# Kernel optimization log

Hardware: AMD Instinct MI355X
Metric: run time of the kernel (lower is better)

Reference implementation:

```python
import jax, jax.numpy as jnp
import numpy as np

B, T, N, D, H, K, L = 16, 32, 128, 128, 128, 2, 2
M = K + 1  # one support (laplacian) * K diffusion steps + identity


def setup_inputs() -> dict:
    key = jax.random.key(0)
    ks = jax.random.split(key, 8)
    std = 0.05
    Din = D + H  # layer-0 concat dim (== H+H for layer 1 since D==H)
    return {
        "inputs": jax.random.normal(ks[0], (B, T, N, D), jnp.float32),
        "initial_hidden_state": jnp.zeros((L, B, N * H), jnp.float32),
        # row-stochastic-ish dynamic supports, scaled for stable diffusion
        "supports": jax.random.uniform(ks[1], (1, T, N, N), jnp.float32) / N,
        "Wg0": jax.random.normal(ks[2], (Din * M, 2 * H), jnp.float32) * std,
        "bg0": jnp.ones((2 * H,), jnp.float32),  # bias_start=1.0 for gates
        "Wc0": jax.random.normal(ks[3], (Din * M, H), jnp.float32) * std,
        "bc0": jnp.zeros((H,), jnp.float32),
        "Wg1": jax.random.normal(ks[4], ((H + H) * M, 2 * H), jnp.float32) * std,
        "bg1": jnp.ones((2 * H,), jnp.float32),
        "Wc1": jax.random.normal(ks[5], ((H + H) * M, H), jnp.float32) * std,
        "bc1": jnp.zeros((H,), jnp.float32),
    }


def _dconv(sup, x, W, b):
    """Diffusion graph conv. sup: [S,N,N]; x: [B,N,Dcat] -> [B,N,out].
    Chebyshev recurrence x2 = 2*S@x1 - x0, per the original DCGRU cell.
    Feature layout matches torch code: last axis is (Dcat, num_matrices)."""
    xs = [x]
    for s in range(sup.shape[0]):
        x0 = x
        x1 = jnp.einsum('mn,bnd->bmd', sup[s], x)
        xs.append(x1)
        for _ in range(2, K + 1):
            x2 = 2.0 * jnp.einsum('mn,bnd->bmd', sup[s], x1) - x0
            xs.append(x2)
            x0, x1 = x1, x2
    xc = jnp.stack(xs, axis=-1).reshape(x.shape[0], x.shape[1], -1)  # [B,N,Dcat*M]
    return jnp.einsum('bnd,do->bno', xc, W) + b


def _dcgru_forward(inputs, initial_hidden_state, supports, params):
    # inputs: [B,T,N,D] -> [T,B,N*D]
    x_seq = jnp.transpose(inputs, (1, 0, 2, 3)).reshape(T, B, N * D)
    sup_seq = jnp.transpose(supports, (1, 0, 2, 3))  # [T,S,N,N]
    cur = x_seq
    finals = []
    for i in range(L):
        Wg, bg, Wc, bc = params[i]

        def step(h, xt_sup, Wg=Wg, bg=bg, Wc=Wc, bc=bc):
            xt, sup = xt_sup
            xin = xt.reshape(B, N, -1)
            hm = h.reshape(B, N, H)
            gates = jax.nn.sigmoid(_dconv(sup, jnp.concatenate([xin, hm], -1), Wg, bg))
            r, u = jnp.split(gates, 2, axis=-1)
            c = jnp.tanh(_dconv(sup, jnp.concatenate([xin, r * hm], -1), Wc, bc))
            hn = (u * hm + (1.0 - u) * c).reshape(B, N * H)
            return hn, hn

        h_last, outs = jax.lax.scan(step, initial_hidden_state[i], (cur, sup_seq))
        finals.append(h_last)
        cur = outs
    return jnp.stack(finals, axis=0), cur  # ([L,B,N*H], [T,B,N*H])


def reference(inputs, initial_hidden_state, supports,
              Wg0, bg0, Wc0, bc0, Wg1, bg1, Wc1, bc1):
    params = [(Wg0, bg0, Wc0, bc0), (Wg1, bg1, Wc1, bc1)]
    return _dcgru_forward(inputs, initial_hidden_state, supports, params)
```

## Files before the change

### kernel.cpp

```cpp
#include <hip/hip_runtime.h>
#include <math.h>


typedef __attribute__((ext_vector_type(8))) short bf16x8;
typedef __attribute__((ext_vector_type(4))) float f32x4;

namespace {
constexpr int GD = 256, NTHR = 1024;
constexpr int CTW = 136;
constexpr int BFW = 776;
}

__device__ __forceinline__ unsigned short f2bf(float x) {
  unsigned u = __float_as_uint(x);
  u += 0x7fff + ((u >> 16) & 1);
  return (unsigned short)(u >> 16);
}
__device__ __forceinline__ float bf2f(unsigned hw) {
  return __uint_as_float(hw << 16);
}

__device__ __forceinline__ void grid_barrier(unsigned* bar) {
  __syncthreads();
  if (threadIdx.x == 0) {
    unsigned* cnt = bar;
    unsigned* gen = bar + 32;
    unsigned g = __hip_atomic_load(gen, __ATOMIC_RELAXED, __HIP_MEMORY_SCOPE_AGENT);
    unsigned a = __hip_atomic_fetch_add(cnt, 1u, __ATOMIC_ACQ_REL, __HIP_MEMORY_SCOPE_AGENT);
    if (a == (unsigned)(GD - 1)) {
      __hip_atomic_store(cnt, 0u, __ATOMIC_RELAXED, __HIP_MEMORY_SCOPE_AGENT);
      __hip_atomic_fetch_add(gen, 1u, __ATOMIC_ACQ_REL, __HIP_MEMORY_SCOPE_AGENT);
    } else {
      while (__hip_atomic_load(gen, __ATOMIC_ACQUIRE, __HIP_MEMORY_SCOPE_AGENT) == g) {
        __builtin_amdgcn_s_sleep(1);
      }
    }
  }
  __syncthreads();
}

__device__ __forceinline__ void diffusion(
    int bid, int tid, int s, const float* __restrict__ inputs,
    const float* __restrict__ seqs, const float* __restrict__ hsrc_base,
    const unsigned short* __restrict__ Sfr,
    unsigned short* __restrict__ D1g, unsigned short* __restrict__ D2g,
    unsigned short* lds) {
  const int layer = bid >> 7;
  const int t = layer ? (s - 1) : s;
  const bool act = layer ? (s >= 1) : (s < 32);
  if (!act) return;
  const int b = (bid >> 3) & 15, fs = (bid & 7) * 32;
  const int lane = tid & 63, w = tid >> 6, quad = lane >> 4, l16 = lane & 15;
  unsigned short* catT = lds;
  unsigned short* D1T  = lds + 32 * CTW;

  for (int p = tid; p < 2048; p += NTHR) {
    const int f = p & 31, n2 = (p >> 5) << 1;
    float v0, v1;
    if (fs < 128) {
      const float* xb = (layer == 0)
          ? inputs + (long)((b * 32 + t) * 128) * 128
          : seqs + (long)(t & 1) * 262144 + (long)(b * 128) * 128;
      v0 = xb[n2 * 128 + fs + f];
      v1 = xb[(n2 + 1) * 128 + fs + f];
    } else {
      const float* hb = hsrc_base + (long)(layer * 2048 + b * 128) * 128;
      v0 = hb[n2 * 128 + (fs - 128) + f];
      v1 = hb[(n2 + 1) * 128 + (fs - 128) + f];
    }
    *(unsigned*)(catT + f * CTW + n2) =
        (unsigned)f2bf(v0) | ((unsigned)f2bf(v1) << 16);
  }
  __syncthreads();

  const int mt = w >> 1, ft = w & 1;
  const unsigned short* Sb = Sfr + (long)t * 16384;

  f32x4 acc = {0.f, 0.f, 0.f, 0.f};
#pragma unroll
  for (int ks = 0; ks < 4; ks++) {
    bf16x8 a = *(const bf16x8*)(Sb + (((mt * 4 + ks) * 64) + lane) * 8);
    bf16x8 bb = *(const bf16x8*)(catT + (ft * 16 + l16) * CTW + ks * 32 + quad * 8);
    acc = __builtin_amdgcn_mfma_f32_16x16x32_bf16(a, bb, acc, 0, 0, 0);
  }
  {
    unsigned short* dst = D1T + (ft * 16 + l16) * CTW + mt * 16 + quad * 4;
    const unsigned lo = (unsigned)f2bf(acc[0]) | ((unsigned)f2bf(acc[1]) << 16);
    const unsigned hi = (unsigned)f2bf(acc[2]) | ((unsigned)f2bf(acc[3]) << 16);
    *(uint2*)dst = make_uint2(lo, hi);
  }
  __syncthreads();

  f32x4 acc2 = {0.f, 0.f, 0.f, 0.f};
#pragma unroll
  for (int ks = 0; ks < 4; ks++) {
    bf16x8 a = *(const bf16x8*)(Sb + (((mt * 4 + ks) * 64) + lane) * 8);
    bf16x8 bb = *(const bf16x8*)(D1T + (ft * 16 + l16) * CTW + ks * 32 + quad * 8);
    acc2 = __builtin_amdgcn_mfma_f32_16x16x32_bf16(a, bb, acc2, 0, 0, 0);
  }
  {
    unsigned short* cp = catT + (ft * 16 + l16) * CTW + mt * 16 + quad * 4;
    const uint2 cv = *(const uint2*)cp;
    const float d0 = 2.f * acc2[0] - bf2f(cv.x & 0xffffu);
    const float d1 = 2.f * acc2[1] - bf2f(cv.x >> 16);
    const float d2 = 2.f * acc2[2] - bf2f(cv.y & 0xffffu);
    const float d3 = 2.f * acc2[3] - bf2f(cv.y >> 16);
    const unsigned lo = (unsigned)f2bf(d0) | ((unsigned)f2bf(d1) << 16);
    const unsigned hi = (unsigned)f2bf(d2) | ((unsigned)f2bf(d3) << 16);
    *(uint2*)cp = make_uint2(lo, hi);
  }
  __syncthreads();

  {
    const int m = tid >> 3, f4 = (tid & 7) << 2;
    const long row = (long)(layer * 2048 + b * 128 + m);
    unsigned lo = (unsigned)D1T[(f4 + 0) * CTW + m] |
                  ((unsigned)D1T[(f4 + 1) * CTW + m] << 16);
    unsigned hi = (unsigned)D1T[(f4 + 2) * CTW + m] |
                  ((unsigned)D1T[(f4 + 3) * CTW + m] << 16);
    *(uint2*)(D1g + row * 256 + fs + f4) = make_uint2(lo, hi);
    lo = (unsigned)catT[(f4 + 0) * CTW + m] |
         ((unsigned)catT[(f4 + 1) * CTW + m] << 16);
    hi = (unsigned)catT[(f4 + 2) * CTW + m] |
         ((unsigned)catT[(f4 + 3) * CTW + m] << 16);
    *(uint2*)(D2g + row * 256 + fs + f4) = make_uint2(lo, hi);
  }
}

__global__ void __launch_bounds__(NTHR, 1) dcgru(
    const float* __restrict__ inputs, const float* __restrict__ init_h,
    const float* __restrict__ sup,
    const float* __restrict__ Wg0, const float* __restrict__ bg0,
    const float* __restrict__ Wc0, const float* __restrict__ bc0,
    const float* __restrict__ Wg1, const float* __restrict__ bg1,
    const float* __restrict__ Wc1, const float* __restrict__ bc1,
    float* __restrict__ out, void* __restrict__ wsv) {
  __shared__ unsigned short LDS[16 * BFW];

  unsigned* bar = (unsigned*)wsv;
  float* h_ws  = (float*)wsv + 64;
  float* rh_ws = h_ws + 524288;
  float* uu_ws = rh_ws + 524288;
  float* seqs  = uu_ws + 524288;
  unsigned short* D1g = (unsigned short*)(seqs + 524288);
  unsigned short* D2g = D1g + 1048576;
  unsigned short* Sfr = D2g + 1048576;
  unsigned short* Wbg = Sfr + 524288;
  unsigned short* Wbc = Wbg + 393216;

  const int tid = threadIdx.x, bid = blockIdx.x;
  const int gtid = bid * NTHR + tid, gstride = GD * NTHR;
  const int lane = tid & 63, w = tid >> 6, quad = lane >> 4, l16 = lane & 15;

  for (int i = gtid; i < 524288; i += gstride) h_ws[i] = init_h[i];
  for (int idx = gtid; idx < 65536; idx += gstride) {
    const int t = idx >> 11, mt = (idx >> 8) & 7, ks = (idx >> 6) & 3, ln = idx & 63;
    const int m = mt * 16 + (ln & 15), k0 = ks * 32 + (ln >> 4) * 8;
    const float* src = sup + (long)t * 16384 + m * 128 + k0;
    bf16x8 v;
#pragma unroll
    for (int j = 0; j < 8; j++) v[j] = (short)f2bf(src[j]);
    *(bf16x8*)(Sfr + (long)idx * 8) = v;
  }
  for (int idx = gtid; idx < 49152; idx += gstride) {
    const int l = idx / 24576;
    int rem = idx - l * 24576;
    const int ot = rem / 1536; rem -= ot * 1536;
    const int ks = rem >> 6, ln = rem & 63;
    const int o = ot * 16 + (ln & 15);
    const float* W = l ? Wg1 : Wg0;
    bf16x8 v;
#pragma unroll
    for (int j = 0; j < 8; j++) {
      const int kk = ks * 32 + (ln >> 4) * 8 + j;
      const int mm = kk >> 8, d = kk & 255;
      v[j] = (short)f2bf(W[(d * 3 + mm) * 256 + o]);
    }
    *(bf16x8*)(Wbg + (long)idx * 8) = v;
  }
  for (int idx = gtid; idx < 24576; idx += gstride) {
    const int l = idx / 12288;
    int rem = idx - l * 12288;
    const int ot = rem / 1536; rem -= ot * 1536;
    const int ks = rem >> 6, ln = rem & 63;
    const int o = ot * 16 + (ln & 15);
    const float* W = l ? Wc1 : Wc0;
    bf16x8 v;
#pragma unroll
    for (int j = 0; j < 8; j++) {
      const int kk = ks * 32 + (ln >> 4) * 8 + j;
      const int mm = kk >> 8, d = kk & 255;
      v[j] = (short)f2bf(W[(d * 3 + mm) * 128 + o]);
    }
    *(bf16x8*)(Wbc + (long)idx * 8) = v;
  }
  grid_barrier(bar);

  for (int s = 0; s < 33; s++) {
    diffusion(bid, tid, s, inputs, seqs, h_ws, Sfr, D1g, D2g, LDS);
    grid_barrier(bar);

    {
      const int row0 = bid * 16;
      const int layer = row0 >> 11;
      const int t = layer ? (s - 1) : s;
      const bool act = layer ? (s >= 1) : (s < 32);
      if (act) {
        for (int p = tid; p < 6144; p += NTHR) {
          const int rr = p / 384, k2 = (p - rr * 384) << 1;
          const int row = row0 + rr, r2 = row & 2047, b = r2 >> 7, n = r2 & 127;
          unsigned pk;
          if (k2 < 256) {
            float2 v;
            if (k2 < 128) {
              v = (layer == 0)
                  ? *(const float2*)&inputs[(long)((b * 32 + t) * 128 + n) * 128 + k2]
                  : *(const float2*)&seqs[(long)(t & 1) * 262144 + (long)r2 * 128 + k2];
            } else {
              v = *(const float2*)&h_ws[(long)row * 128 + (k2 - 128)];
            }
            pk = (unsigned)f2bf(v.x) | ((unsigned)f2bf(v.y) << 16);
          } else if (k2 < 512) {
            pk = *(const unsigned*)(D1g + (long)row * 256 + (k2 - 256));
          } else {
            pk = *(const unsigned*)(D2g + (long)row * 256 + (k2 - 512));
          }
          *(unsigned*)(LDS + rr * BFW + k2) = pk;
        }
        __syncthreads();
        f32x4 acc = {0.f, 0.f, 0.f, 0.f};
        const unsigned short* Wb = Wbg + ((long)(layer * 16 + w) * 24) * 512;
        for (int ks = 0; ks < 24; ks++) {
          bf16x8 a = *(const bf16x8*)(LDS + l16 * BFW + ks * 32 + quad * 8);
          bf16x8 bb = *(const bf16x8*)(Wb + ks * 512 + lane * 8);
          acc = __builtin_amdgcn_mfma_f32_16x16x32_bf16(a, bb, acc, 0, 0, 0);
        }
        const int o = w * 16 + l16;
        const float bias = (layer ? bg1 : bg0)[o];
#pragma unroll
        for (int r = 0; r < 4; r++) {
          const int row = row0 + quad * 4 + r;
          const float g = 1.f / (1.f + __expf(-(acc[r] + bias)));
          if (o < 128) rh_ws[(long)row * 128 + o] = g * h_ws[(long)row * 128 + o];
          else         uu_ws[(long)row * 128 + (o - 128)] = g;
        }
      }
    }
    grid_barrier(bar);

    diffusion(bid, tid, s, inputs, seqs, rh_ws, Sfr, D1g, D2g, LDS);
    grid_barrier(bar);

    {
      const int row0 = bid * 16;
      const int layer = row0 >> 11;
      const int t = layer ? (s - 1) : s;
      const bool act = layer ? (s >= 1) : (s < 32);
      if (act) {
        for (int p = tid; p < 6144; p += NTHR) {
          const int rr = p / 384, k2 = (p - rr * 384) << 1;
          const int row = row0 + rr, r2 = row & 2047, b = r2 >> 7, n = r2 & 127;
          unsigned pk;
          if (k2 < 256) {
            float2 v;
            if (k2 < 128) {
              v = (layer == 0)
                  ? *(const float2*)&inputs[(long)((b * 32 + t) * 128 + n) * 128 + k2]
                  : *(const float2*)&seqs[(long)(t & 1) * 262144 + (long)r2 * 128 + k2];
            } else {
              v = *(const float2*)&rh_ws[(long)row * 128 + (k2 - 128)];
            }
            pk = (unsigned)f2bf(v.x) | ((unsigned)f2bf(v.y) << 16);
          } else if (k2 < 512) {
            pk = *(const unsigned*)(D1g + (long)row * 256 + (k2 - 256));
          } else {
            pk = *(const unsigned*)(D2g + (long)row * 256 + (k2 - 512));
          }
          *(unsigned*)(LDS + rr * BFW + k2) = pk;
        }
        __syncthreads();
        if (w < 8) {
          f32x4 acc = {0.f, 0.f, 0.f, 0.f};
          const unsigned short* Wb = Wbc + ((long)(layer * 8 + w) * 24) * 512;
          for (int ks = 0; ks < 24; ks++) {
            bf16x8 a = *(const bf16x8*)(LDS + l16 * BFW + ks * 32 + quad * 8);
            bf16x8 bb = *(const bf16x8*)(Wb + ks * 512 + lane * 8);
            acc = __builtin_amdgcn_mfma_f32_16x16x32_bf16(a, bb, acc, 0, 0, 0);
          }
          const int o = w * 16 + l16;
          const float bias = (layer ? bc1 : bc0)[o];
#pragma unroll
          for (int r = 0; r < 4; r++) {
            const int row = row0 + quad * 4 + r, r2 = row & 2047;
            const float cv = tanhf(acc[r] + bias);
            const float uv = uu_ws[(long)row * 128 + o];
            const float hv = h_ws[(long)row * 128 + o];
            const float hn = uv * hv + (1.f - uv) * cv;
            h_ws[(long)row * 128 + o] = hn;
            if (layer == 0) {
              seqs[(long)(s & 1) * 262144 + (long)r2 * 128 + o] = hn;
              if (t == 31) out[(long)r2 * 128 + o] = hn;
            } else {
              out[524288 + (long)t * 262144 + (long)r2 * 128 + o] = hn;
              if (t == 31) out[262144 + (long)r2 * 128 + o] = hn;
            }
          }
        }
      }
    }
    grid_barrier(bar);
  }
}

extern "C" void kernel_launch(void* const* d_in, const int* in_sizes, int n_in,
                              void* d_out, int out_size, void* d_ws, size_t ws_size,
                              hipStream_t stream) {
  const float* inputs = (const float*)d_in[0];
  const float* init_h = (const float*)d_in[1];
  const float* sup    = (const float*)d_in[2];
  const float* Wg0 = (const float*)d_in[3];
  const float* bg0 = (const float*)d_in[4];
  const float* Wc0 = (const float*)d_in[5];
  const float* bc0 = (const float*)d_in[6];
  const float* Wg1 = (const float*)d_in[7];
  const float* bg1 = (const float*)d_in[8];
  const float* Wc1 = (const float*)d_in[9];
  const float* bc1 = (const float*)d_in[10];
  float* out = (float*)d_out;

  hipMemsetAsync(d_ws, 0, 256, stream);
  dcgru<<<GD, NTHR, 0, stream>>>(inputs, init_h, sup, Wg0, bg0, Wc0, bc0,
                                 Wg1, bg1, Wc1, bc1, out, d_ws);
}
```

Before: 3.601 ms.

## Assign one block per (layer,batch) and keep hidden state in LDS

The grid shrinks from 256 to 32 blocks. Each block now owns one (layer, batch) pair and runs both diffusions and both gate GEMMs for it locally. The hidden state stays resident in LDS, and the per-step grid barriers drop from four to one, since each block produces its own diffusion inputs. This uses XOR-swizzled LDS layouts and larger per-wave MFMA tiles. The trade is that only 32 CUs do all the work, so much less of the GPU is used in parallel.

```diff
diff --git a/kernel.cpp b/kernel.cpp
--- a/kernel.cpp
+++ b/kernel.cpp
@@ -6,9 +6,7 @@
 typedef __attribute__((ext_vector_type(4))) float f32x4;
 
 namespace {
-constexpr int GD = 256, NTHR = 1024;
-constexpr int CTW = 136;
-constexpr int BFW = 776;
+constexpr int GD = 32, NTHR = 1024;
 }
 
 __device__ __forceinline__ unsigned short f2bf(float x) {
@@ -18,6 +16,15 @@
 }
 __device__ __forceinline__ float bf2f(unsigned hw) {
   return __uint_as_float(hw << 16);
+}
+__device__ __forceinline__ unsigned pk2(float a, float b) {
+  return (unsigned)f2bf(a) | ((unsigned)f2bf(b) << 16);
+}
+__device__ __forceinline__ int BIdx(int r, int c) {
+  return (r << 7) + (c ^ ((r & 7) << 3));
+}
+__device__ __forceinline__ int HsIdx(int n, int f) {
+  return (n << 7) + (f ^ (n & 31));
 }
 
 __device__ __forceinline__ void grid_barrier(unsigned* bar) {
@@ -39,95 +46,97 @@
   __syncthreads();
 }
 
-__device__ __forceinline__ void diffusion(
-    int bid, int tid, int s, const float* __restrict__ inputs,
-    const float* __restrict__ seqs, const float* __restrict__ hsrc_base,
-    const unsigned short* __restrict__ Sfr,
-    unsigned short* __restrict__ D1g, unsigned short* __restrict__ D2g,
-    unsigned short* lds) {
-  const int layer = bid >> 7;
-  const int t = layer ? (s - 1) : s;
-  const bool act = layer ? (s >= 1) : (s < 32);
-  if (!act) return;
-  const int b = (bid >> 3) & 15, fs = (bid & 7) * 32;
-  const int lane = tid & 63, w = tid >> 6, quad = lane >> 4, l16 = lane & 15;
-  unsigned short* catT = lds;
-  unsigned short* D1T  = lds + 32 * CTW;
-
-  for (int p = tid; p < 2048; p += NTHR) {
-    const int f = p & 31, n2 = (p >> 5) << 1;
-    float v0, v1;
-    if (fs < 128) {
-      const float* xb = (layer == 0)
-          ? inputs + (long)((b * 32 + t) * 128) * 128
-          : seqs + (long)(t & 1) * 262144 + (long)(b * 128) * 128;
-      v0 = xb[n2 * 128 + fs + f];
-      v1 = xb[(n2 + 1) * 128 + fs + f];
+__device__ __forceinline__ void diff_half(
+    const unsigned short* __restrict__ Sb, const unsigned short* Bt,
+    const unsigned short* Ct, unsigned short* Ot,
+    unsigned short* __restrict__ Dg, int dbase,
+    int w, int lane, int quad, int l16) {
+  const int mtg = w >> 2, ftg = w & 3;
+  f32x4 acc[2][2];
+#pragma unroll
+  for (int mi = 0; mi < 2; ++mi)
+#pragma unroll
+    for (int fi = 0; fi < 2; ++fi) acc[mi][fi] = (f32x4){0.f, 0.f, 0.f, 0.f};
+#pragma unroll
+  for (int ks = 0; ks < 4; ++ks) {
+    bf16x8 a[2], bb[2];
+#pragma unroll
+    for (int mi = 0; mi < 2; ++mi)
+      a[mi] = *(const bf16x8*)(Sb + (((mtg * 2 + mi) * 4 + ks) * 64 + lane) * 8);
+#pragma unroll
+    for (int fi = 0; fi < 2; ++fi)
+      bb[fi] = *(const bf16x8*)(Bt + BIdx((ftg * 2 + fi) * 16 + l16, ks * 32 + quad * 8));
+#pragma unroll
+    for (int mi = 0; mi < 2; ++mi)
+#pragma unroll
+      for (int fi = 0; fi < 2; ++fi)
+        acc[mi][fi] =
+            __builtin_amdgcn_mfma_f32_16x16x32_bf16(a[mi], bb[fi], acc[mi][fi], 0, 0, 0);
+  }
+#pragma unroll
+  for (int mi = 0; mi < 2; ++mi)
+#pragma unroll
+    for (int fi = 0; fi < 2; ++fi) {
+      const int f = (ftg * 2 + fi) * 16 + l16;
+      const int m0 = (mtg * 2 + mi) * 16 + quad * 4;
+      float v0 = acc[mi][fi][0], v1 = acc[mi][fi][1];
+      float v2 = acc[mi][fi][2], v3 = acc[mi][fi][3];
+      if (Ct) {
+        const uint2 cv = *(const uint2*)(Ct + BIdx(f, m0));
+        v0 = 2.f * v0 - bf2f(cv.x & 0xffffu);
+        v1 = 2.f * v1 - bf2f(cv.x >> 16);
+        v2 = 2.f * v2 - bf2f(cv.y & 0xffffu);
+        v3 = 2.f * v3 - bf2f(cv.y >> 16);
+      }
+      if (Ot) *(uint2*)(Ot + BIdx(f, m0)) = make_uint2(pk2(v0, v1), pk2(v2, v3));
+      const int d = dbase + f;
+      Dg[(m0 + 0) * 256 + (d ^ (((m0 + 0) & 7) << 3))] = f2bf(v0);
+      Dg[(m0 + 1) * 256 + (d ^ (((m0 + 1) & 7) << 3))] = f2bf(v1);
+      Dg[(m0 + 2) * 256 + (d ^ (((m0 + 2) & 7) << 3))] = f2bf(v2);
+      Dg[(m0 + 3) * 256 + (d ^ (((m0 + 3) & 7) << 3))] = f2bf(v3);
+    }
+}
+
+__device__ __forceinline__ void stage_chunk(
+    int c, bool gates, int tid, const float* __restrict__ xsrc,
+    const float* Hsp, const unsigned short* W2p, unsigned short* W1p,
+    const unsigned short* __restrict__ D1b, const unsigned short* __restrict__ D2b) {
+  if (c == 0) {
+    const int row = tid >> 3, cb = (tid & 7) << 4;
+#pragma unroll
+    for (int j = 0; j < 4; ++j) {
+      const float4 v = *(const float4*)(xsrc + row * 128 + cb + j * 4);
+      *(uint2*)(W1p + BIdx(row, cb + j * 4)) = make_uint2(pk2(v.x, v.y), pk2(v.z, v.w));
+    }
+  } else if (c == 1) {
+    if (gates) {
+      const int row = tid >> 3, cb = (tid & 7) << 4;
+#pragma unroll
+      for (int j = 0; j < 8; ++j) {
+        const float v0 = Hsp[HsIdx(row, cb + 2 * j)];
+        const float v1 = Hsp[HsIdx(row, cb + 2 * j + 1)];
+        *(unsigned*)(W1p + BIdx(row, cb + 2 * j)) = pk2(v0, v1);
+      }
     } else {
-      const float* hb = hsrc_base + (long)(layer * 2048 + b * 128) * 128;
-      v0 = hb[n2 * 128 + (fs - 128) + f];
-      v1 = hb[(n2 + 1) * 128 + (fs - 128) + f];
-    }
-    *(unsigned*)(catT + f * CTW + n2) =
-        (unsigned)f2bf(v0) | ((unsigned)f2bf(v1) << 16);
-  }
-  __syncthreads();
-
-  const int mt = w >> 1, ft = w & 1;
-  const unsigned short* Sb = Sfr + (long)t * 16384;
-
-  f32x4 acc = {0.f, 0.f, 0.f, 0.f};
-#pragma unroll
-  for (int ks = 0; ks < 4; ks++) {
-    bf16x8 a = *(const bf16x8*)(Sb + (((mt * 4 + ks) * 64) + lane) * 8);
-    bf16x8 bb = *(const bf16x8*)(catT + (ft * 16 + l16) * CTW + ks * 32 + quad * 8);
-    acc = __builtin_amdgcn_mfma_f32_16x16x32_bf16(a, bb, acc, 0, 0, 0);
-  }
-  {
-    unsigned short* dst = D1T + (ft * 16 + l16) * CTW + mt * 16 + quad * 4;
-    const unsigned lo = (unsigned)f2bf(acc[0]) | ((unsigned)f2bf(acc[1]) << 16);
-    const unsigned hi = (unsigned)f2bf(acc[2]) | ((unsigned)f2bf(acc[3]) << 16);
-    *(uint2*)dst = make_uint2(lo, hi);
-  }
-  __syncthreads();
-
-  f32x4 acc2 = {0.f, 0.f, 0.f, 0.f};
-#pragma unroll
-  for (int ks = 0; ks < 4; ks++) {
-    bf16x8 a = *(const bf16x8*)(Sb + (((mt * 4 + ks) * 64) + lane) * 8);
-    bf16x8 bb = *(const bf16x8*)(D1T + (ft * 16 + l16) * CTW + ks * 32 + quad * 8);
-    acc2 = __builtin_amdgcn_mfma_f32_16x16x32_bf16(a, bb, acc2, 0, 0, 0);
-  }
-  {
-    unsigned short* cp = catT + (ft * 16 + l16) * CTW + mt * 16 + quad * 4;
-    const uint2 cv = *(const uint2*)cp;
-    const float d0 = 2.f * acc2[0] - bf2f(cv.x & 0xffffu);
-    const float d1 = 2.f * acc2[1] - bf2f(cv.x >> 16);
-    const float d2 = 2.f * acc2[2] - bf2f(cv.y & 0xffffu);
-    const float d3 = 2.f * acc2[3] - bf2f(cv.y >> 16);
-    const unsigned lo = (unsigned)f2bf(d0) | ((unsigned)f2bf(d1) << 16);
-    const unsigned hi = (unsigned)f2bf(d2) | ((unsigned)f2bf(d3) << 16);
-    *(uint2*)cp = make_uint2(lo, hi);
-  }
-  __syncthreads();
-
-  {
-    const int m = tid >> 3, f4 = (tid & 7) << 2;
-    const long row = (long)(layer * 2048 + b * 128 + m);
-    unsigned lo = (unsigned)D1T[(f4 + 0) * CTW + m] |
-                  ((unsigned)D1T[(f4 + 1) * CTW + m] << 16);
-    unsigned hi = (unsigned)D1T[(f4 + 2) * CTW + m] |
-                  ((unsigned)D1T[(f4 + 3) * CTW + m] << 16);
-    *(uint2*)(D1g + row * 256 + fs + f4) = make_uint2(lo, hi);
-    lo = (unsigned)catT[(f4 + 0) * CTW + m] |
-         ((unsigned)catT[(f4 + 1) * CTW + m] << 16);
-    hi = (unsigned)catT[(f4 + 2) * CTW + m] |
-         ((unsigned)catT[(f4 + 3) * CTW + m] << 16);
-    *(uint2*)(D2g + row * 256 + fs + f4) = make_uint2(lo, hi);
-  }
-}
-
-__global__ void __launch_bounds__(NTHR, 1) dcgru(
+      const int m = tid & 127, db = (tid >> 7) << 4;
+      unsigned short tmp[16];
+#pragma unroll
+      for (int j = 0; j < 16; ++j) tmp[j] = W2p[BIdx(db + j, m)];
+#pragma unroll
+      for (int j = 0; j < 8; ++j)
+        *(unsigned*)(W1p + BIdx(m, db + 2 * j)) =
+            (unsigned)tmp[2 * j] | ((unsigned)tmp[2 * j + 1] << 16);
+    }
+  } else {
+    const unsigned short* src = ((c < 4) ? D1b : D2b) + ((c & 1) ? 128 : 0);
+    const int row = tid >> 3, cb = (tid & 7) << 4;
+    const unsigned short* srow = src + row * 256;
+    *(uint4*)(W1p + row * 128 + cb) = *(const uint4*)(srow + cb);
+    *(uint4*)(W1p + row * 128 + cb + 8) = *(const uint4*)(srow + cb + 8);
+  }
+}
+
+__global__ void __launch_bounds__(NTHR, 4) dcgru(
     const float* __restrict__ inputs, const float* __restrict__ init_h,
     const float* __restrict__ sup,
     const float* __restrict__ Wg0, const float* __restrict__ bg0,
@@ -135,14 +144,14 @@
     const float* __restrict__ Wg1, const float* __restrict__ bg1,
     const float* __restrict__ Wc1, const float* __restrict__ bc1,
     float* __restrict__ out, void* __restrict__ wsv) {
-  __shared__ unsigned short LDS[16 * BFW];
+  __shared__ float Hs[16384];
+  __shared__ unsigned short W1[16384];
+  __shared__ unsigned short W2[16384];
 
   unsigned* bar = (unsigned*)wsv;
-  float* h_ws  = (float*)wsv + 64;
-  float* rh_ws = h_ws + 524288;
-  float* uu_ws = rh_ws + 524288;
-  float* seqs  = uu_ws + 524288;
-  unsigned short* D1g = (unsigned short*)(seqs + 524288);
+  float* seqs = (float*)wsv + 64;
+  float* u_ws = seqs + 524288;
+  unsigned short* D1g = (unsigned short*)(u_ws + 524288);
   unsigned short* D2g = D1g + 1048576;
   unsigned short* Sfr = D2g + 1048576;
   unsigned short* Wbg = Sfr + 524288;
@@ -151,12 +160,18 @@
   const int tid = threadIdx.x, bid = blockIdx.x;
   const int gtid = bid * NTHR + tid, gstride = GD * NTHR;
   const int lane = tid & 63, w = tid >> 6, quad = lane >> 4, l16 = lane & 15;
-
-  for (int i = gtid; i < 524288; i += gstride) h_ws[i] = init_h[i];
+  const int layer = bid >> 4, b = bid & 15;
+
+  float* u_blk = u_ws + (long)bid * 16384;
+  unsigned short* D1b = D1g + (long)bid * 32768;
+  unsigned short* D2b = D2g + (long)bid * 32768;
+
+  for (int i = tid; i < 16384; i += NTHR)
+    Hs[HsIdx(i >> 7, i & 127)] = init_h[(long)(layer * 16 + b) * 16384 + i];
   for (int idx = gtid; idx < 65536; idx += gstride) {
-    const int t = idx >> 11, mt = (idx >> 8) & 7, ks = (idx >> 6) & 3, ln = idx & 63;
+    const int tt = idx >> 11, mt = (idx >> 8) & 7, ks = (idx >> 6) & 3, ln = idx & 63;
     const int m = mt * 16 + (ln & 15), k0 = ks * 32 + (ln >> 4) * 8;
-    const float* src = sup + (long)t * 16384 + m * 128 + k0;
+    const float* src = sup + (long)tt * 16384 + m * 128 + k0;
     bf16x8 v;
 #pragma unroll
     for (int j = 0; j < 8; j++) v[j] = (short)f2bf(src[j]);
@@ -196,115 +211,169 @@
   }
   grid_barrier(bar);
 
-  for (int s = 0; s < 33; s++) {
-    diffusion(bid, tid, s, inputs, seqs, h_ws, Sfr, D1g, D2g, LDS);
-    grid_barrier(bar);
-
-    {
-      const int row0 = bid * 16;
-      const int layer = row0 >> 11;
-      const int t = layer ? (s - 1) : s;
-      const bool act = layer ? (s >= 1) : (s < 32);
-      if (act) {
-        for (int p = tid; p < 6144; p += NTHR) {
-          const int rr = p / 384, k2 = (p - rr * 384) << 1;
-          const int row = row0 + rr, r2 = row & 2047, b = r2 >> 7, n = r2 & 127;
-          unsigned pk;
-          if (k2 < 256) {
-            float2 v;
-            if (k2 < 128) {
-              v = (layer == 0)
-                  ? *(const float2*)&inputs[(long)((b * 32 + t) * 128 + n) * 128 + k2]
-                  : *(const float2*)&seqs[(long)(t & 1) * 262144 + (long)r2 * 128 + k2];
-            } else {
-              v = *(const float2*)&h_ws[(long)row * 128 + (k2 - 128)];
-            }
-            pk = (unsigned)f2bf(v.x) | ((unsigned)f2bf(v.y) << 16);
-          } else if (k2 < 512) {
-            pk = *(const unsigned*)(D1g + (long)row * 256 + (k2 - 256));
+  const float* bgL = layer ? bg1 : bg0;
+  const float* bcL = layer ? bc1 : bc0;
+
+  for (int s = 0; s < 33; ++s) {
+    const int t = layer ? (s - 1) : s;
+    const bool act = layer ? (s >= 1) : (s < 32);
+    if (act) {
+      const float* xsrc = (layer == 0)
+          ? inputs + (long)(b * 32 + t) * 16384
+          : seqs + (long)(t & 1) * 262144 + (long)b * 16384;
+      const unsigned short* Sb = Sfr + (long)t * 16384;
+
+      for (int fh = 0; fh < 2; ++fh) {
+#pragma unroll
+        for (int it = 0; it < 8; ++it) {
+          const int f = it * 16 + (tid >> 6), n2 = (tid & 63) << 1;
+          float v0, v1;
+          if (fh == 0) {
+            v0 = xsrc[n2 * 128 + f];
+            v1 = xsrc[(n2 + 1) * 128 + f];
           } else {
-            pk = *(const unsigned*)(D2g + (long)row * 256 + (k2 - 512));
+            v0 = Hs[HsIdx(n2, f)];
+            v1 = Hs[HsIdx(n2 + 1, f)];
           }
-          *(unsigned*)(LDS + rr * BFW + k2) = pk;
+          *(unsigned*)(W1 + BIdx(f, n2)) = pk2(v0, v1);
         }
         __syncthreads();
-        f32x4 acc = {0.f, 0.f, 0.f, 0.f};
-        const unsigned short* Wb = Wbg + ((long)(layer * 16 + w) * 24) * 512;
-        for (int ks = 0; ks < 24; ks++) {
-          bf16x8 a = *(const bf16x8*)(LDS + l16 * BFW + ks * 32 + quad * 8);
-          bf16x8 bb = *(const bf16x8*)(Wb + ks * 512 + lane * 8);
-          acc = __builtin_amdgcn_mfma_f32_16x16x32_bf16(a, bb, acc, 0, 0, 0);
+        diff_half(Sb, W1, nullptr, W2, D1b, fh * 128, w, lane, quad, l16);
+        __syncthreads();
+        diff_half(Sb, W2, W1, nullptr, D2b, fh * 128, w, lane, quad, l16);
+        __syncthreads();
+      }
+
+      {
+        f32x4 acc[4][4];
+#pragma unroll
+        for (int mi = 0; mi < 4; ++mi)
+#pragma unroll
+          for (int oj = 0; oj < 4; ++oj) acc[mi][oj] = (f32x4){0.f, 0.f, 0.f, 0.f};
+        const int rg = w >> 2, cg = w & 3;
+        for (int c = 0; c < 6; ++c) {
+          stage_chunk(c, true, tid, xsrc, Hs, W2, W1, D1b, D2b);
+          __syncthreads();
+          if (w < 8) {
+#pragma unroll
+            for (int ks = 0; ks < 4; ++ks) {
+              bf16x8 a[4], bb[4];
+#pragma unroll
+              for (int mi = 0; mi < 4; ++mi)
+                a[mi] = *(const bf16x8*)(W1 + BIdx(rg * 64 + mi * 16 + l16, ks * 32 + quad * 8));
+#pragma unroll
+              for (int oj = 0; oj < 4; ++oj)
+                bb[oj] = *(const bf16x8*)(Wbg +
+                    ((long)((layer * 16 + cg * 4 + oj) * 24 + c * 4 + ks)) * 512 + lane * 8);
+#pragma unroll
+              for (int mi = 0; mi < 4; ++mi)
+#pragma unroll
+                for (int oj = 0; oj < 4; ++oj)
+                  acc[mi][oj] = __builtin_amdgcn_mfma_f32_16x16x32_bf16(
+                      a[mi], bb[oj], acc[mi][oj], 0, 0, 0);
+            }
+          }
+          __syncthreads();
         }
-        const int o = w * 16 + l16;
-        const float bias = (layer ? bg1 : bg0)[o];
-#pragma unroll
-        for (int r = 0; r < 4; r++) {
-          const int row = row0 + quad * 4 + r;
-          const float g = 1.f / (1.f + __expf(-(acc[r] + bias)));
-          if (o < 128) rh_ws[(long)row * 128 + o] = g * h_ws[(long)row * 128 + o];
-          else         uu_ws[(long)row * 128 + (o - 128)] = g;
-        }
-      }
-    }
-    grid_barrier(bar);
-
-    diffusion(bid, tid, s, inputs, seqs, rh_ws, Sfr, D1g, D2g, LDS);
-    grid_barrier(bar);
-
-    {
-      const int row0 = bid * 16;
-      const int layer = row0 >> 11;
-      const int t = layer ? (s - 1) : s;
-      const bool act = layer ? (s >= 1) : (s < 32);
-      if (act) {
-        for (int p = tid; p < 6144; p += NTHR) {
-          const int rr = p / 384, k2 = (p - rr * 384) << 1;
-          const int row = row0 + rr, r2 = row & 2047, b = r2 >> 7, n = r2 & 127;
-          unsigned pk;
-          if (k2 < 256) {
-            float2 v;
-            if (k2 < 128) {
-              v = (layer == 0)
-                  ? *(const float2*)&inputs[(long)((b * 32 + t) * 128 + n) * 128 + k2]
-                  : *(const float2*)&seqs[(long)(t & 1) * 262144 + (long)r2 * 128 + k2];
-            } else {
-              v = *(const float2*)&rh_ws[(long)row * 128 + (k2 - 128)];
-            }
-            pk = (unsigned)f2bf(v.x) | ((unsigned)f2bf(v.y) << 16);
-          } else if (k2 < 512) {
-            pk = *(const unsigned*)(D1g + (long)row * 256 + (k2 - 256));
+        if (w < 8) {
+          if (cg < 2) {
+#pragma unroll
+            for (int mi = 0; mi < 4; ++mi)
+#pragma unroll
+              for (int oj = 0; oj < 4; ++oj) {
+                const int o = cg * 64 + oj * 16 + l16;
+                const float bias = bgL[o];
+                const int m0 = rg * 64 + mi * 16 + quad * 4;
+                float rh[4];
+#pragma unroll
+                for (int r = 0; r < 4; ++r) {
+                  const float g = 1.f / (1.f + __expf(-(acc[mi][oj][r] + bias)));
+                  rh[r] = g * Hs[HsIdx(m0 + r, o)];
+                }
+                *(uint2*)(W2 + BIdx(o, m0)) =
+                    make_uint2(pk2(rh[0], rh[1]), pk2(rh[2], rh[3]));
+              }
           } else {
-            pk = *(const unsigned*)(D2g + (long)row * 256 + (k2 - 512));
+#pragma unroll
+            for (int mi = 0; mi < 4; ++mi)
+#pragma unroll
+              for (int oj = 0; oj < 4; ++oj) {
+                const int og = cg * 64 + oj * 16 + l16;
+                const float bias = bgL[og];
+                const int m0 = rg * 64 + mi * 16 + quad * 4;
+#pragma unroll
+                for (int r = 0; r < 4; ++r) {
+                  const float g = 1.f / (1.f + __expf(-(acc[mi][oj][r] + bias)));
+                  u_blk[(m0 + r) * 128 + (og - 128)] = g;
+                }
+              }
           }
-          *(unsigned*)(LDS + rr * BFW + k2) = pk;
         }
         __syncthreads();
-        if (w < 8) {
-          f32x4 acc = {0.f, 0.f, 0.f, 0.f};
-          const unsigned short* Wb = Wbc + ((long)(layer * 8 + w) * 24) * 512;
-          for (int ks = 0; ks < 24; ks++) {
-            bf16x8 a = *(const bf16x8*)(LDS + l16 * BFW + ks * 32 + quad * 8);
-            bf16x8 bb = *(const bf16x8*)(Wb + ks * 512 + lane * 8);
-            acc = __builtin_amdgcn_mfma_f32_16x16x32_bf16(a, bb, acc, 0, 0, 0);
-          }
-          const int o = w * 16 + l16;
-          const float bias = (layer ? bc1 : bc0)[o];
-#pragma unroll
-          for (int r = 0; r < 4; r++) {
-            const int row = row0 + quad * 4 + r, r2 = row & 2047;
-            const float cv = tanhf(acc[r] + bias);
-            const float uv = uu_ws[(long)row * 128 + o];
-            const float hv = h_ws[(long)row * 128 + o];
-            const float hn = uv * hv + (1.f - uv) * cv;
-            h_ws[(long)row * 128 + o] = hn;
-            if (layer == 0) {
-              seqs[(long)(s & 1) * 262144 + (long)r2 * 128 + o] = hn;
-              if (t == 31) out[(long)r2 * 128 + o] = hn;
-            } else {
-              out[524288 + (long)t * 262144 + (long)r2 * 128 + o] = hn;
-              if (t == 31) out[262144 + (long)r2 * 128 + o] = hn;
+      }
+
+      diff_half(Sb, W2, nullptr, W1, D1b, 128, w, lane, quad, l16);
+      __syncthreads();
+      diff_half(Sb, W1, W2, nullptr, D2b, 128, w, lane, quad, l16);
+      __syncthreads();
+
+      {
+        f32x4 acc[4][4];
+#pragma unroll
+        for (int mi = 0; mi < 4; ++mi)
+#pragma unroll
+          for (int oj = 0; oj < 4; ++oj) acc[mi][oj] = (f32x4){0.f, 0.f, 0.f, 0.f};
+        const int rg = w >> 1, cg = w & 1;
+        for (int c = 0; c < 6; ++c) {
+          stage_chunk(c, false, tid, xsrc, Hs, W2, W1, D1b, D2b);
+          __syncthreads();
+          if (w < 4) {
+#pragma unroll
+            for (int ks = 0; ks < 4; ++ks) {
+              bf16x8 a[4], bb[4];
+#pragma unroll
+              for (int mi = 0; mi < 4; ++mi)
+                a[mi] = *(const bf16x8*)(W1 + BIdx(rg * 64 + mi * 16 + l16, ks * 32 + quad * 8));
+#pragma unroll
+              for (int oj = 0; oj < 4; ++oj)
+                bb[oj] = *(const bf16x8*)(Wbc +
+                    ((long)((layer * 8 + cg * 4 + oj) * 24 + c * 4 + ks)) * 512 + lane * 8);
+#pragma unroll
+              for (int mi = 0; mi < 4; ++mi)
+#pragma unroll
+                for (int oj = 0; oj < 4; ++oj)
+                  acc[mi][oj] = __builtin_amdgcn_mfma_f32_16x16x32_bf16(
+                      a[mi], bb[oj], acc[mi][oj], 0, 0, 0);
             }
           }
+          __syncthreads();
+        }
+        if (w < 4) {
+#pragma unroll
+          for (int mi = 0; mi < 4; ++mi)
+#pragma unroll
+            for (int oj = 0; oj < 4; ++oj) {
+              const int o = cg * 64 + oj * 16 + l16;
+              const float bias = bcL[o];
+              const int m0 = rg * 64 + mi * 16 + quad * 4;
+#pragma unroll
+              for (int r = 0; r < 4; ++r) {
+                const int m = m0 + r;
+                const float cv = tanhf(acc[mi][oj][r] + bias);
+                const float uv = u_blk[m * 128 + o];
+                const float hv = Hs[HsIdx(m, o)];
+                const float hn = uv * hv + (1.f - uv) * cv;
+                Hs[HsIdx(m, o)] = hn;
+                const long base = (long)(b * 128 + m) * 128 + o;
+                if (layer == 0) {
+                  seqs[(long)(s & 1) * 262144 + base] = hn;
+                  if (t == 31) out[base] = hn;
+                } else {
+                  out[524288 + (long)t * 262144 + base] = hn;
+                  if (t == 31) out[262144 + base] = hn;
+                }
+              }
+            }
         }
       }
     }
```

New measurement: 7.235 ms. +100.9%, slower.
